# Optimization experiments

Hardware: AMD Instinct MI355X
Metric: run time of the kernel (lower is better)

The kernel has to match this reference:

```python
import jax, jax.numpy as jnp
import numpy as np

D_MODEL = 512
NHEAD = 8
HEAD_DIM = D_MODEL // NHEAD
NS = 1  # num_special_tokens


def setup_inputs() -> dict:
    key = jax.random.key(0)
    ks = jax.random.split(key, 12)
    B, N = 8, 1024
    x = jax.random.normal(ks[0], (B, N, D_MODEL), dtype=jnp.float32)
    coords = jax.random.normal(ks[1], (B, N, 3), dtype=jnp.float32) * 5.0
    key_padding_mask = jnp.zeros((B, N), dtype=bool)
    s = 1.0 / np.sqrt(D_MODEL)
    qkv_w = jax.random.normal(ks[2], (3 * D_MODEL, D_MODEL), dtype=jnp.float32) * s
    out_w = jax.random.normal(ks[3], (D_MODEL, D_MODEL), dtype=jnp.float32) * s
    out_b = jnp.zeros((D_MODEL,), dtype=jnp.float32)
    bias_alpha = jnp.ones((1,), dtype=jnp.float32) * 0.5  # nonzero so bias path matters
    w1 = jax.random.normal(ks[4], (NHEAD * 4, 4), dtype=jnp.float32) * 0.5
    b1 = jnp.zeros((NHEAD * 4,), dtype=jnp.float32)
    w2 = jax.random.normal(ks[5], (NHEAD, NHEAD * 4), dtype=jnp.float32) * 0.2
    b2 = jnp.zeros((NHEAD,), dtype=jnp.float32)
    coord_scales = jnp.array([12.0, 12.0, 5.0], dtype=jnp.float32)
    return dict(x=x, coords=coords, key_padding_mask=key_padding_mask,
                qkv_w=qkv_w, out_w=out_w, out_b=out_b, bias_alpha=bias_alpha,
                w1=w1, b1=b1, w2=w2, b2=b2, coord_scales=coord_scales)


def reference(x, coords, key_padding_mask, qkv_w, out_w, out_b, bias_alpha,
              w1, b1, w2, b2, coord_scales):
    B, N, _ = x.shape
    scale = HEAD_DIM ** (-0.5)
    qkv = x @ qkv_w.T  # [B,N,3D]
    q, k, v = jnp.split(qkv, 3, axis=-1)
    def heads(t):
        return t.reshape(B, N, NHEAD, HEAD_DIM).transpose(0, 2, 1, 3)  # [B,H,N,dh]
    q, k, v = heads(q), heads(k), heads(v)

    c = coords / coord_scales  # [B,N,3]
    dpos = c[:, :, None, :] - c[:, None, :, :]  # [B,N,N,3]
    dist = jnp.linalg.norm(dpos, axis=-1, keepdims=True)  # [B,N,N,1]
    feat = jnp.concatenate([dpos, dist], axis=-1)  # [B,N,N,4]
    h = jax.nn.gelu(feat @ w1.T + b1, approximate=False)  # [B,N,N,4H]
    bias = (h @ w2.T + b2).transpose(0, 3, 1, 2)  # [B,H,N,N]
    # zero out bias rows/cols for special tokens
    bias = bias.at[:, :, :NS, :].set(0.0)
    bias = bias.at[:, :, :, :NS].set(0.0)

    dots = jnp.einsum('bhid,bhjd->bhij', q, k) * scale
    logits = dots + bias_alpha * bias
    logits = jnp.where(key_padding_mask[:, None, None, :], -1e30, logits)
    attn = jax.nn.softmax(logits, axis=-1)
    out = jnp.einsum('bhij,bhjd->bhid', attn, v)
    out = out.transpose(0, 2, 1, 3).reshape(B, N, D_MODEL)
    return out @ out_w.T + out_b
```

## Files before the change

kernel.cpp:

```cpp
#include <hip/hip_runtime.h>
#include <math.h>

#define D_MODEL 512
#define NHEAD   8
#define HEAD_DIM 64
#define BB      8
#define NN      1024
#define NS      1
#define TI      16
#define TJ      32
#define NT      (NN / TJ)
#define FIX_M   10.0f
#define GSTRIDE 40

typedef __attribute__((ext_vector_type(8))) short short8;
typedef __attribute__((ext_vector_type(4))) float floatx4;

__device__ __forceinline__ float gelu_fast(float x) {
    const float s = x * 0.70710678118654752f;
    const float u = fabsf(s);
    const float t = __builtin_amdgcn_rcpf(fmaf(0.3275911f, u, 1.0f));
    float p = fmaf(1.061405429f, t, -1.453152027f);
    p = fmaf(p, t, 1.421413741f);
    p = fmaf(p, t, -0.284496736f);
    p = fmaf(p, t, 0.254829592f);
    p = p * t;
    const float e = __expf(-u * u);
    float erf_u = fmaf(-p, e, 1.0f);
    erf_u = copysignf(erf_u, s);
    return 0.5f * x * (1.0f + erf_u);
}

__device__ __forceinline__ unsigned short f2bf(float f) {
    unsigned u = __float_as_uint(f);
    u = (u + 0x7fffu + ((u >> 16) & 1u)) >> 16;
    return (unsigned short)u;
}

__device__ __forceinline__ uint2 pack4bf(float a, float b, float c, float d) {
    uint2 p;
    p.x = (unsigned)f2bf(a) | ((unsigned)f2bf(b) << 16);
    p.y = (unsigned)f2bf(c) | ((unsigned)f2bf(d) << 16);
    return p;
}

__global__ __launch_bounds__(256)
void gemm_qkv_mfma(const float* __restrict__ A, const float* __restrict__ Bm,
                   unsigned short* __restrict__ Qb, unsigned short* __restrict__ Kb,
                   unsigned short* __restrict__ Vt) {
    __shared__ __align__(16) unsigned short As[128 * GSTRIDE];
    __shared__ __align__(16) unsigned short Bs[128 * GSTRIDE];
    const int tid = threadIdx.x;
    const int bm = blockIdx.y * 128;
    const int bn = blockIdx.x * 128;
    const int wv = tid >> 6, lane = tid & 63, quad = lane >> 4, ln = lane & 15;
    const int wm = (wv >> 1) * 64, wn = (wv & 1) * 64;

    floatx4 acc[4][4];
    #pragma unroll
    for (int i = 0; i < 4; ++i)
        #pragma unroll
        for (int j = 0; j < 4; ++j) acc[i][j] = (floatx4){0.f, 0.f, 0.f, 0.f};

    for (int k0 = 0; k0 < 512; k0 += 32) {
        __syncthreads();
        #pragma unroll
        for (int t = 0; t < 4; ++t) {
            const int c = tid + t * 256;
            const int row = c >> 3, kc = (c & 7) * 4;
            float4 v = *(const float4*)(A + (size_t)(bm + row) * 512 + k0 + kc);
            *(uint2*)&As[row * GSTRIDE + kc] = pack4bf(v.x, v.y, v.z, v.w);
            float4 w = *(const float4*)(Bm + (size_t)(bn + row) * 512 + k0 + kc);
            *(uint2*)&Bs[row * GSTRIDE + kc] = pack4bf(w.x, w.y, w.z, w.w);
        }
        __syncthreads();
        short8 af[4], bf[4];
        #pragma unroll
        for (int mb = 0; mb < 4; ++mb)
            af[mb] = *(const short8*)&As[(wm + mb * 16 + ln) * GSTRIDE + quad * 8];
        #pragma unroll
        for (int nb = 0; nb < 4; ++nb)
            bf[nb] = *(const short8*)&Bs[(wn + nb * 16 + ln) * GSTRIDE + quad * 8];
        #pragma unroll
        for (int mb = 0; mb < 4; ++mb)
            #pragma unroll
            for (int nb = 0; nb < 4; ++nb)
                acc[mb][nb] = __builtin_amdgcn_mfma_f32_16x16x32_bf16(af[mb], bf[nb], acc[mb][nb], 0, 0, 0);
    }

    #pragma unroll
    for (int nb = 0; nb < 4; ++nb) {
        const int n = bn + wn + nb * 16 + ln;
        #pragma unroll
        for (int mb = 0; mb < 4; ++mb) {
            const int m = bm + wm + mb * 16 + quad * 4;
            if (n < 512) {
                #pragma unroll
                for (int r = 0; r < 4; ++r)
                    Qb[(size_t)(m + r) * 512 + n] = f2bf(acc[mb][nb][r] * 0.125f);
            } else if (n < 1024) {
                #pragma unroll
                for (int r = 0; r < 4; ++r)
                    Kb[(size_t)(m + r) * 512 + (n - 512)] = f2bf(acc[mb][nb][r]);
            } else {
                const int bb = m >> 10, tok = m & 1023;
                *(uint2*)(Vt + ((size_t)bb * 512 + (n - 1024)) * NN + tok) =
                    pack4bf(acc[mb][nb][0], acc[mb][nb][1], acc[mb][nb][2], acc[mb][nb][3]);
            }
        }
    }
}

__global__ __launch_bounds__(256)
void gemm_out_mfma(const unsigned short* __restrict__ Ab, const float* __restrict__ Bm,
                   const float* __restrict__ bias, float* __restrict__ C) {
    __shared__ __align__(16) unsigned short As[128 * GSTRIDE];
    __shared__ __align__(16) unsigned short Bs[128 * GSTRIDE];
    const int tid = threadIdx.x;
    const int bm = blockIdx.y * 128;
    const int bn = blockIdx.x * 128;
    const int wv = tid >> 6, lane = tid & 63, quad = lane >> 4, ln = lane & 15;
    const int wm = (wv >> 1) * 64, wn = (wv & 1) * 64;

    floatx4 acc[4][4];
    #pragma unroll
    for (int i = 0; i < 4; ++i)
        #pragma unroll
        for (int j = 0; j < 4; ++j) acc[i][j] = (floatx4){0.f, 0.f, 0.f, 0.f};

    for (int k0 = 0; k0 < 512; k0 += 32) {
        __syncthreads();
        #pragma unroll
        for (int t = 0; t < 4; ++t) {
            const int c = tid + t * 256;
            const int row = c >> 3, kc = (c & 7) * 4;
            *(uint2*)&As[row * GSTRIDE + kc] =
                *(const uint2*)(Ab + (size_t)(bm + row) * 512 + k0 + kc);
            float4 w = *(const float4*)(Bm + (size_t)(bn + row) * 512 + k0 + kc);
            *(uint2*)&Bs[row * GSTRIDE + kc] = pack4bf(w.x, w.y, w.z, w.w);
        }
        __syncthreads();
        short8 af[4], bf[4];
        #pragma unroll
        for (int mb = 0; mb < 4; ++mb)
            af[mb] = *(const short8*)&As[(wm + mb * 16 + ln) * GSTRIDE + quad * 8];
        #pragma unroll
        for (int nb = 0; nb < 4; ++nb)
            bf[nb] = *(const short8*)&Bs[(wn + nb * 16 + ln) * GSTRIDE + quad * 8];
        #pragma unroll
        for (int mb = 0; mb < 4; ++mb)
            #pragma unroll
            for (int nb = 0; nb < 4; ++nb)
                acc[mb][nb] = __builtin_amdgcn_mfma_f32_16x16x32_bf16(af[mb], bf[nb], acc[mb][nb], 0, 0, 0);
    }

    #pragma unroll
    for (int nb = 0; nb < 4; ++nb) {
        const int n = bn + wn + nb * 16 + ln;
        const float bv = bias[n];
        #pragma unroll
        for (int mb = 0; mb < 4; ++mb) {
            const int m = bm + wm + mb * 16 + quad * 4;
            #pragma unroll
            for (int r = 0; r < 4; ++r)
                C[(size_t)(m + r) * 512 + n] = acc[mb][nb][r] + bv;
        }
    }
}

#define BIAS_IDX(i, j, h) ((i) * 291 + (j) * 9 + (h))
__global__ __launch_bounds__(256, 2)
void attn_kernel(const unsigned short* __restrict__ Qb,
                 const unsigned short* __restrict__ Kb,
                 const unsigned short* __restrict__ Vt,
                 const float* __restrict__ coords,
                 const unsigned char* __restrict__ mask,
                 const float* __restrict__ w1, const float* __restrict__ b1,
                 const float* __restrict__ w2, const float* __restrict__ b2,
                 const float* __restrict__ coord_scales,
                 const float* __restrict__ alpha_p,
                 unsigned short* __restrict__ attn_out) {
    const int b   = blockIdx.y;
    const int i0  = blockIdx.x * TI;
    const int tid = threadIdx.x;
    const int wv  = tid >> 6;
    const int lane = tid & 63;
    const int quad = lane >> 4;
    const int ln   = lane & 15;
    const int h0   = wv * 2;

    __shared__ float bias_s[2][TI * 291 + 9];
    __shared__ __align__(16) unsigned short ps[NHEAD][TI][40];
    __shared__ float ci_s[TI][3];

    const float alpha = alpha_p[0];
    const float isx = 1.0f / coord_scales[0];
    const float isy = 1.0f / coord_scales[1];
    const float isz = 1.0f / coord_scales[2];

    if (tid < TI * 3)
        ci_s[tid / 3][tid % 3] =
            coords[((size_t)b * NN + i0 + tid / 3) * 3 + tid % 3] / coord_scales[tid % 3];

    float4 w1r[8]; float b1r[8];
    #pragma unroll
    for (int jj = 0; jj < 8; ++jj) {
        w1r[jj] = *(const float4*)(w1 + (quad * 8 + jj) * 4);
        b1r[jj] = b1[quad * 8 + jj];
    }
    short8 b2f;
    #pragma unroll
    for (int jj = 0; jj < 8; ++jj) {
        const float v = (ln < 8) ? alpha * w2[ln * 32 + quad * 8 + jj] : 0.0f;
        b2f[jj] = (short)f2bf(v);
    }
    const float ab2 = (ln < 8) ? alpha * b2[ln] : 0.0f;

    short8 qf[2][2];
    #pragma unroll
    for (int hh = 0; hh < 2; ++hh)
        #pragma unroll
        for (int kd = 0; kd < 2; ++kd)
            qf[hh][kd] = *(const short8*)(Qb + ((size_t)b * NN + i0 + ln) * 512
                                          + (h0 + hh) * 64 + kd * 32 + quad * 8);

    floatx4 oacc[2][4];
    #pragma unroll
    for (int hh = 0; hh < 2; ++hh)
        #pragma unroll
        for (int nd = 0; nd < 4; ++nd)
            oacc[hh][nd] = (floatx4){0.f, 0.f, 0.f, 0.f};
    float l_part[2][4];
    #pragma unroll
    for (int hh = 0; hh < 2; ++hh)
        #pragma unroll
        for (int r = 0; r < 4; ++r) l_part[hh][r] = 0.f;

    const unsigned char* maskp = mask + (size_t)b * NN;
    float cjx[2], cjy[2], cjz[2];

    #define LOAD_CJ(tt_) do { const int tt = (tt_);                               \
        if (tt < NT) {                                                            \
            const float* cp0 = coords + ((size_t)b * NN + tt * TJ + ln) * 3;      \
            cjx[0] = cp0[0] * isx; cjy[0] = cp0[1] * isy; cjz[0] = cp0[2] * isz;  \
            cjx[1] = cp0[48] * isx; cjy[1] = cp0[49] * isy; cjz[1] = cp0[50] * isz; \
        } } while (0)

    #define MLP_TILE(tt_) do { const int tt = (tt_);                              \
        if (tt < NT) {                                                            \
            float* bout = bias_s[tt & 1];                                         \
            const int j0m = tt * TJ;                                              \
            _Pragma("unroll")                                                     \
            for (int g = 0; g < 4; ++g) {                                         \
                const int i = wv * 4 + g;                                         \
                const float cix = ci_s[i][0], ciy = ci_s[i][1], ciz = ci_s[i][2]; \
                const bool irow0 = (i0 + i < NS);                                 \
                _Pragma("unroll")                                                 \
                for (int jh = 0; jh < 2; ++jh) {                                  \
                    const float dx = cix - cjx[jh];                               \
                    const float dy = ciy - cjy[jh];                               \
                    const float dz = ciz - cjz[jh];                               \
                    const float dist = sqrtf(dx * dx + dy * dy + dz * dz);        \
                    short8 hf;                                                    \
                    _Pragma("unroll")                                             \
                    for (int jj = 0; jj < 8; ++jj) {                              \
                        const float4 wa = w1r[jj];                                \
                        float hu = fmaf(wa.x, dx, fmaf(wa.y, dy,                  \
                                   fmaf(wa.z, dz, fmaf(wa.w, dist, b1r[jj]))));   \
                        hu = gelu_fast(hu);                                       \
                        hf[jj] = (short)f2bf(hu);                                 \
                    }                                                             \
                    floatx4 D = __builtin_amdgcn_mfma_f32_16x16x32_bf16(          \
                        hf, b2f, (floatx4){0.f, 0.f, 0.f, 0.f}, 0, 0, 0);         \
                    if (ln < 8) {                                                 \
                        _Pragma("unroll")                                         \
                        for (int r = 0; r < 4; ++r) {                             \
                            const int jw = jh * 16 + quad * 4 + r;                \
                            const float val = (irow0 || (j0m + jw < NS))          \
                                              ? 0.0f : (D[r] + ab2);              \
                            bout[BIAS_IDX(i, jw, ln)] = val;                      \
                        }                                                         \
                    }                                                             \
                }                                                                 \
            }                                                                     \
        } } while (0)

    __syncthreads();
    LOAD_CJ(0);
    MLP_TILE(0);
    __syncthreads();

    for (int jt = 0; jt < NT; ++jt) {
        const int j0 = jt * TJ;
        const int pb = jt & 1;

        short8 kf[2][4], vf[2][4];
        #pragma unroll
        for (int hh = 0; hh < 2; ++hh) {
            const unsigned short* kbase = Kb + ((size_t)b * NN + j0) * 512 + (h0 + hh) * 64;
            kf[hh][0] = *(const short8*)(kbase + (size_t)ln * 512 + quad * 8);
            kf[hh][1] = *(const short8*)(kbase + (size_t)ln * 512 + 32 + quad * 8);
            kf[hh][2] = *(const short8*)(kbase + (size_t)(16 + ln) * 512 + quad * 8);
            kf[hh][3] = *(const short8*)(kbase + (size_t)(16 + ln) * 512 + 32 + quad * 8);
            const unsigned short* vbase = Vt + ((size_t)b * 512 + (h0 + hh) * 64) * NN + j0 + quad * 8;
            #pragma unroll
            for (int nd = 0; nd < 4; ++nd)
                vf[hh][nd] = *(const short8*)(vbase + (size_t)(nd * 16 + ln) * NN);
        }
        const unsigned char mm0 = maskp[j0 + ln];
        const unsigned char mm1 = maskp[j0 + 16 + ln];

        LOAD_CJ(jt + 1);
        MLP_TILE(jt + 1);

        #pragma unroll
        for (int hh = 0; hh < 2; ++hh) {
            const int h = h0 + hh;
            floatx4 s0 = (floatx4){0.f, 0.f, 0.f, 0.f};
            floatx4 s1 = (floatx4){0.f, 0.f, 0.f, 0.f};
            s0 = __builtin_amdgcn_mfma_f32_16x16x32_bf16(qf[hh][0], kf[hh][0], s0, 0, 0, 0);
            s0 = __builtin_amdgcn_mfma_f32_16x16x32_bf16(qf[hh][1], kf[hh][1], s0, 0, 0, 0);
            s1 = __builtin_amdgcn_mfma_f32_16x16x32_bf16(qf[hh][0], kf[hh][2], s1, 0, 0, 0);
            s1 = __builtin_amdgcn_mfma_f32_16x16x32_bf16(qf[hh][1], kf[hh][3], s1, 0, 0, 0);
            #pragma unroll
            for (int r = 0; r < 4; ++r) {
                const int row = quad * 4 + r;
                float v0 = s0[r] + bias_s[pb][BIAS_IDX(row, ln, h)];
                float v1 = s1[r] + bias_s[pb][BIAS_IDX(row, 16 + ln, h)];
                v0 = mm0 ? -1e30f : v0;
                v1 = mm1 ? -1e30f : v1;
                const float e0 = __expf(v0 - FIX_M);
                const float e1 = __expf(v1 - FIX_M);
                l_part[hh][r] += e0 + e1;
                ps[h][row][ln]      = f2bf(e0);
                ps[h][row][16 + ln] = f2bf(e1);
            }
        }

        #pragma unroll
        for (int hh = 0; hh < 2; ++hh) {
            const int h = h0 + hh;
            short8 pa = *(const short8*)&ps[h][ln][quad * 8];
            #pragma unroll
            for (int nd = 0; nd < 4; ++nd)
                oacc[hh][nd] = __builtin_amdgcn_mfma_f32_16x16x32_bf16(pa, vf[hh][nd], oacc[hh][nd], 0, 0, 0);
        }

        __syncthreads();
    }

    #pragma unroll
    for (int hh = 0; hh < 2; ++hh) {
        float rl[4];
        #pragma unroll
        for (int r = 0; r < 4; ++r) {
            float l = l_part[hh][r];
            l += __shfl_xor(l, 1, 64);
            l += __shfl_xor(l, 2, 64);
            l += __shfl_xor(l, 4, 64);
            l += __shfl_xor(l, 8, 64);
            rl[r] = 1.0f / l;
        }
        #pragma unroll
        for (int nd = 0; nd < 4; ++nd)
            #pragma unroll
            for (int r = 0; r < 4; ++r)
                attn_out[((size_t)b * NN + i0 + quad * 4 + r) * 512
                         + (h0 + hh) * 64 + nd * 16 + ln] = f2bf(oacc[hh][nd][r] * rl[r]);
    }
    #undef LOAD_CJ
    #undef MLP_TILE
}

extern "C" void kernel_launch(void* const* d_in, const int* in_sizes, int n_in,
                              void* d_out, int out_size, void* d_ws, size_t ws_size,
                              hipStream_t stream) {
    const float* x        = (const float*)d_in[0];
    const float* coords   = (const float*)d_in[1];
    const unsigned char* kpm = (const unsigned char*)d_in[2];
    const float* qkv_w    = (const float*)d_in[3];
    const float* out_w    = (const float*)d_in[4];
    const float* out_b    = (const float*)d_in[5];
    const float* alpha    = (const float*)d_in[6];
    const float* w1       = (const float*)d_in[7];
    const float* b1       = (const float*)d_in[8];
    const float* w2       = (const float*)d_in[9];
    const float* b2       = (const float*)d_in[10];
    const float* cscales  = (const float*)d_in[11];
    float* out = (float*)d_out;

    const int M = BB * NN;
    unsigned short* Qb = (unsigned short*)d_ws;
    unsigned short* Kb = Qb + (size_t)M * D_MODEL;
    unsigned short* Vt = Kb + (size_t)M * D_MODEL;
    unsigned short* Ao = Vt + (size_t)M * D_MODEL;

    {
        dim3 grid(3 * D_MODEL / 128, M / 128);
        gemm_qkv_mfma<<<grid, 256, 0, stream>>>(x, qkv_w, Qb, Kb, Vt);
    }
    {
        dim3 grid(NN / TI, BB);
        attn_kernel<<<grid, 256, 0, stream>>>(Qb, Kb, Vt, coords, kpm, w1, b1, w2, b2,
                                              cscales, alpha, Ao);
    }
    {
        dim3 grid(D_MODEL / 128, M / 128);
        gemm_out_mfma<<<grid, 256, 0, stream>>>(Ao, out_w, out_b, out);
    }
}
```

Measured before the change: 422.3 us.

## Store pair bias in bf16 LDS, use packed bf16 converts, keep query coords in registers

New measurement: 412.8 us. 1.02x faster.

```diff
diff --git a/kernel.cpp b/kernel.cpp
--- a/kernel.cpp
+++ b/kernel.cpp
@@ -1,4 +1,5 @@
 #include <hip/hip_runtime.h>
+#include <hip/hip_bf16.h>
 #include <math.h>
 
 #define D_MODEL 512
@@ -35,6 +36,10 @@
     unsigned u = __float_as_uint(f);
     u = (u + 0x7fffu + ((u >> 16) & 1u)) >> 16;
     return (unsigned short)u;
+}
+
+__device__ __forceinline__ float bf2f(unsigned short v) {
+    return __uint_as_float(((unsigned)v) << 16);
 }
 
 __device__ __forceinline__ uint2 pack4bf(float a, float b, float c, float d) {
@@ -189,18 +194,20 @@
     const int ln   = lane & 15;
     const int h0   = wv * 2;
 
-    __shared__ float bias_s[2][TI * 291 + 9];
+    __shared__ unsigned short bias_s[2][TI * 291 + 9];
     __shared__ __align__(16) unsigned short ps[NHEAD][TI][40];
-    __shared__ float ci_s[TI][3];
 
     const float alpha = alpha_p[0];
     const float isx = 1.0f / coord_scales[0];
     const float isy = 1.0f / coord_scales[1];
     const float isz = 1.0f / coord_scales[2];
 
-    if (tid < TI * 3)
-        ci_s[tid / 3][tid % 3] =
-            coords[((size_t)b * NN + i0 + tid / 3) * 3 + tid % 3] / coord_scales[tid % 3];
+    float cir[4][3];
+    #pragma unroll
+    for (int g = 0; g < 4; ++g) {
+        const float* cp = coords + ((size_t)b * NN + i0 + wv * 4 + g) * 3;
+        cir[g][0] = cp[0] * isx; cir[g][1] = cp[1] * isy; cir[g][2] = cp[2] * isz;
+    }
 
     float4 w1r[8]; float b1r[8];
     #pragma unroll
@@ -248,12 +255,12 @@
 
     #define MLP_TILE(tt_) do { const int tt = (tt_);                              \
         if (tt < NT) {                                                            \
-            float* bout = bias_s[tt & 1];                                         \
+            unsigned short* bout = bias_s[tt & 1];                                \
             const int j0m = tt * TJ;                                              \
             _Pragma("unroll")                                                     \
             for (int g = 0; g < 4; ++g) {                                         \
                 const int i = wv * 4 + g;                                         \
-                const float cix = ci_s[i][0], ciy = ci_s[i][1], ciz = ci_s[i][2]; \
+                const float cix = cir[g][0], ciy = cir[g][1], ciz = cir[g][2];    \
                 const bool irow0 = (i0 + i < NS);                                 \
                 _Pragma("unroll")                                                 \
                 for (int jh = 0; jh < 2; ++jh) {                                  \
@@ -261,31 +268,36 @@
                     const float dy = ciy - cjy[jh];                               \
                     const float dz = ciz - cjz[jh];                               \
                     const float dist = sqrtf(dx * dx + dy * dy + dz * dz);        \
-                    short8 hf;                                                    \
+                    float hu[8];                                                  \
                     _Pragma("unroll")                                             \
                     for (int jj = 0; jj < 8; ++jj) {                              \
                         const float4 wa = w1r[jj];                                \
-                        float hu = fmaf(wa.x, dx, fmaf(wa.y, dy,                  \
+                        float t0 = fmaf(wa.x, dx, fmaf(wa.y, dy,                  \
                                    fmaf(wa.z, dz, fmaf(wa.w, dist, b1r[jj]))));   \
-                        hu = gelu_fast(hu);                                       \
-                        hf[jj] = (short)f2bf(hu);                                 \
+                        hu[jj] = gelu_fast(t0);                                   \
+                    }                                                             \
+                    union { short8 s8; unsigned u4[4]; } H;                       \
+                    _Pragma("unroll")                                             \
+                    for (int k = 0; k < 4; ++k) {                                 \
+                        __hip_bfloat162 t2 = __float22bfloat162_rn(               \
+                            make_float2(hu[2 * k], hu[2 * k + 1]));               \
+                        H.u4[k] = *(unsigned*)&t2;                                \
                     }                                                             \
                     floatx4 D = __builtin_amdgcn_mfma_f32_16x16x32_bf16(          \
-                        hf, b2f, (floatx4){0.f, 0.f, 0.f, 0.f}, 0, 0, 0);         \
+                        H.s8, b2f, (floatx4){0.f, 0.f, 0.f, 0.f}, 0, 0, 0);       \
                     if (ln < 8) {                                                 \
                         _Pragma("unroll")                                         \
                         for (int r = 0; r < 4; ++r) {                             \
                             const int jw = jh * 16 + quad * 4 + r;                \
                             const float val = (irow0 || (j0m + jw < NS))          \
                                               ? 0.0f : (D[r] + ab2);              \
-                            bout[BIAS_IDX(i, jw, ln)] = val;                      \
+                            bout[BIAS_IDX(i, jw, ln)] = f2bf(val);                \
                         }                                                         \
                     }                                                             \
                 }                                                                 \
             }                                                                     \
         } } while (0)
 
-    __syncthreads();
     LOAD_CJ(0);
     MLP_TILE(0);
     __syncthreads();
@@ -325,8 +337,8 @@
             #pragma unroll
             for (int r = 0; r < 4; ++r) {
                 const int row = quad * 4 + r;
-                float v0 = s0[r] + bias_s[pb][BIAS_IDX(row, ln, h)];
-                float v1 = s1[r] + bias_s[pb][BIAS_IDX(row, 16 + ln, h)];
+                float v0 = s0[r] + bf2f(bias_s[pb][BIAS_IDX(row, ln, h)]);
+                float v1 = s1[r] + bf2f(bias_s[pb][BIAS_IDX(row, 16 + ln, h)]);
                 v0 = mm0 ? -1e30f : v0;
                 v1 = mm1 ? -1e30f : v1;
                 const float e0 = __expf(v0 - FIX_M);
```
